# Kernel tuning notes

Measured on AMD Instinct MI355X. Metric: run time of the kernel, lower is better.

The kernel has to match this reference:

```python
import jax, jax.numpy as jnp
from jax import lax
import numpy as np

EPS = 1e-5
DN = ('NCHW', 'OIHW', 'NCHW')
# Sum of the four Sobel-like kernels used in sobel_conv2d (conv is linear, so
# summing four depthwise convs == one depthwise conv with the summed kernel).
SOBEL_SUM = jnp.array([[2., 4., 4.], [-2., 0., 2.], [-4., -4., -2.]], dtype=jnp.float32)


def conv_bn_relu(x, w, b, g, be, m, v, pad):
    y = lax.conv_general_dilated(x, w, (1, 1), [(pad, pad), (pad, pad)], dimension_numbers=DN)
    y = y + b[None, :, None, None]
    inv = g * lax.rsqrt(v + EPS)
    y = (y - m[None, :, None, None]) * inv[None, :, None, None] + be[None, :, None, None]
    return jax.nn.relu(y)


def sobel_depthwise(x):
    C = x.shape[1]
    k = jnp.broadcast_to(SOBEL_SUM[None, None], (C, 1, 3, 3))
    return lax.conv_general_dilated(x, k, (1, 1), [(1, 1), (1, 1)],
                                    dimension_numbers=DN, feature_group_count=C)


def setup_inputs() -> dict:
    key = jax.random.key(0)
    ks = jax.random.split(key, 20)
    B, Cin, H, W = 16, 64, 128, 128
    Co = 256  # out_channels
    d = {'input_f': jax.random.normal(ks[0], (B, Cin, H, W), jnp.float32)}

    def bn(i, c):
        return (jax.random.normal(ks[i], (c,), jnp.float32) * 0.1 + 1.0,  # gamma
                jax.random.normal(ks[i + 1], (c,), jnp.float32) * 0.1,    # beta
                jax.random.normal(ks[i + 2], (c,), jnp.float32) * 0.1,    # running mean
                jax.random.uniform(ks[i + 3], (c,), jnp.float32, 0.5, 1.5))  # running var

    d['w1'] = jax.random.normal(ks[1], (Co, Cin, 1, 1), jnp.float32) * (1.0 / np.sqrt(Cin))
    d['b1'] = jnp.zeros((Co,), jnp.float32)
    d['g1'], d['be1'], d['m1'], d['v1'] = bn(2, Co)
    d['w2'] = jax.random.normal(ks[6], (Co // 2, Co, 3, 3), jnp.float32) * (1.0 / np.sqrt(Co * 9))
    d['b2'] = jnp.zeros((Co // 2,), jnp.float32)
    d['g2'], d['be2'], d['m2'], d['v2'] = bn(7, Co // 2)
    d['w3'] = jax.random.normal(ks[11], (Co // 4, Co // 2, 3, 3), jnp.float32) * (1.0 / np.sqrt(Co // 2 * 9))
    d['b3'] = jnp.zeros((Co // 4,), jnp.float32)
    d['g3'], d['be3'], d['m3'], d['v3'] = bn(12, Co // 4)
    return d


def reference(input_f, w1, b1, g1, be1, m1, v1, w2, b2, g2, be2, m2, v2,
              w3, b3, g3, be3, m3, v3):
    c1 = conv_bn_relu(input_f, w1, b1, g1, be1, m1, v1, pad=0)  # [B,256,H,W]
    c2 = conv_bn_relu(c1, w2, b2, g2, be2, m2, v2, pad=1)       # [B,128,H,W]
    edge = sobel_depthwise(c2)                                   # [B,128,H,W]
    c3 = conv_bn_relu(edge, w3, b3, g3, be3, m3, v3, pad=1)     # [B,64,H,W]
    return jnp.concatenate([input_f, c3], axis=1)                # [B,128,H,W]
```

## Files before the change

kernel.cpp:

```cpp
#include <hip/hip_runtime.h>

#define HW 16384
#define EPSF 1e-5f

typedef __attribute__((ext_vector_type(8))) short s8v;
typedef __attribute__((ext_vector_type(16))) float f16v;

__device__ __forceinline__ ushort f2b(float f) {
    union { float f; unsigned u; } v; v.f = f;
    return (ushort)((v.u + 0x7FFFu + ((v.u >> 16) & 1u)) >> 16);
}
__device__ __forceinline__ float b2f(ushort h) {
    union { unsigned u; float f; } v; v.u = ((unsigned)h) << 16; return v.f;
}


__global__ void bn_prep(const float* __restrict__ b1, const float* __restrict__ g1,
                        const float* __restrict__ be1, const float* __restrict__ m1,
                        const float* __restrict__ v1,
                        const float* __restrict__ b2, const float* __restrict__ g2,
                        const float* __restrict__ be2, const float* __restrict__ m2,
                        const float* __restrict__ v2,
                        const float* __restrict__ b3, const float* __restrict__ g3,
                        const float* __restrict__ be3, const float* __restrict__ m3,
                        const float* __restrict__ v3,
                        float* __restrict__ ws) {
    int t = threadIdx.x;
    if (t < 256) { float a = g1[t] * rsqrtf(v1[t] + EPSF); ws[t] = a;       ws[256 + t] = (b1[t] - m1[t]) * a + be1[t]; }
    if (t < 128) { float a = g2[t] * rsqrtf(v2[t] + EPSF); ws[512 + t] = a; ws[640 + t] = (b2[t] - m2[t]) * a + be2[t]; }
    if (t < 64)  { float a = g3[t] * rsqrtf(v3[t] + EPSF); ws[768 + t] = a; ws[832 + t] = (b3[t] - m3[t]) * a + be3[t]; }
}

__global__ __launch_bounds__(256) void wprep(const float* __restrict__ w2, const float* __restrict__ w3,
                                             const float* __restrict__ w1,
                                             ushort* __restrict__ w2b, ushort* __restrict__ w3b,
                                             ushort* __restrict__ w1b) {
    int t = blockIdx.x * 256 + threadIdx.x;
    if (t < 9 * 128 * 256) {
        int off = t >> 15; int r = t & 32767; int co = r >> 8; int ci = r & 255;
        w2b[t] = f2b(w2[(co * 256 + ci) * 9 + off]);
    }
    t -= 9 * 128 * 256;
    if (t >= 0 && t < 9 * 64 * 128) {
        int off = t >> 13; int r = t & 8191; int co = r >> 7; int ci = r & 127;
        w3b[t] = f2b(w3[(co * 128 + ci) * 9 + off]);
    }
    t -= 9 * 64 * 128;
    if (t >= 0 && t < 256 * 64) {
        w1b[t] = f2b(w1[t]);
    }
}

__global__ __launch_bounds__(256) void copy_in_k(const float* __restrict__ x, float* __restrict__ out) {
    size_t i = (size_t)blockIdx.x * 256 + threadIdx.x;
    size_t b = i >> 18;
    size_t r = i & 262143;
    ((float4*)out)[b * (size_t)(128 * HW / 4) + r] = ((const float4*)x)[i];
}

__global__ __launch_bounds__(256, 2)
void conv1_mfma(const float* __restrict__ x, const ushort* __restrict__ w1b,
                const float* __restrict__ alpha, const float* __restrict__ beta,
                ushort* __restrict__ c1u, int b0) {
    __shared__ __align__(16) ushort sW[256][72];
    const int tid = threadIdx.x;
    const int lane = tid & 63;
    const int wid = tid >> 6;
    const int l31 = lane & 31;
    const int l5 = lane >> 5;
    const int bz = blockIdx.x >> 7;
    const int y  = blockIdx.x & 127;
    const int px = wid * 32 + l31;

#pragma unroll
    for (int it = 0; it < 8; ++it) {
        const int idx = it * 256 + tid;
        const int co = idx >> 3, cig = idx & 7;
        *(int4*)&sW[co][cig * 8] = *(const int4*)&w1b[co * 64 + cig * 8];
    }

    const float* xp = x + ((size_t)(b0 + bz) * 64 + l5 * 8) * HW + y * 128 + px;
    float xv[32];
#pragma unroll
    for (int s = 0; s < 4; ++s)
#pragma unroll
        for (int j = 0; j < 8; ++j)
            xv[s * 8 + j] = xp[(size_t)(s * 16 + j) * HW];

    union { ushort u[8]; s8v v; } hf[4], lf[4];
#pragma unroll
    for (int s = 0; s < 4; ++s)
#pragma unroll
        for (int j = 0; j < 8; ++j) {
            union { float f; unsigned u; } t0; t0.f = xv[s * 8 + j];
            hf[s].u[j] = (ushort)(t0.u >> 16);
            union { unsigned u; float f; } t1; t1.u = t0.u & 0xFFFF0000u;
            lf[s].u[j] = f2b(t0.f - t1.f);
        }

    f16v acc[8];
#pragma unroll
    for (int ct = 0; ct < 8; ++ct) acc[ct] = (f16v)(0.0f);

    __syncthreads();
#pragma unroll
    for (int s = 0; s < 4; ++s) {
#pragma unroll
        for (int ct = 0; ct < 8; ++ct) {
            const s8v af = *(const s8v*)&sW[ct * 32 + l31][s * 16 + l5 * 8];
            acc[ct] = __builtin_amdgcn_mfma_f32_32x32x16_bf16(af, hf[s].v, acc[ct], 0, 0, 0);
            acc[ct] = __builtin_amdgcn_mfma_f32_32x32x16_bf16(af, lf[s].v, acc[ct], 0, 0, 0);
        }
    }

    const int piece = y >> 6;
    const size_t base = (size_t)(2 * bz + piece) * 4194304 + (size_t)(y & 63) * 128 * 256;
#pragma unroll
    for (int ct = 0; ct < 8; ++ct) {
#pragma unroll
        for (int rg = 0; rg < 4; ++rg) {
            const int co0 = ct * 32 + rg * 8 + l5 * 4;
            const float4 av = *(const float4*)&alpha[co0];
            const float4 bv = *(const float4*)&beta[co0];
            ushort4 o;
            o.x = f2b(fmaxf(acc[ct][rg * 4 + 0] * av.x + bv.x, 0.f));
            o.y = f2b(fmaxf(acc[ct][rg * 4 + 1] * av.y + bv.y, 0.f));
            o.z = f2b(fmaxf(acc[ct][rg * 4 + 2] * av.z + bv.z, 0.f));
            o.w = f2b(fmaxf(acc[ct][rg * 4 + 3] * av.w + bv.w, 0.f));
            *(ushort4*)&c1u[base + (size_t)px * 256 + co0] = o;
        }
    }
}

__global__ __launch_bounds__(256, 2)
void conv2_mfma(const ushort* __restrict__ c1u, const ushort* __restrict__ wb,
                const float* __restrict__ alpha, const float* __restrict__ beta,
                ushort* __restrict__ ybf, int b0) {
    constexpr int CI = 256, CO = 128, MT = 2;
    __shared__ __align__(16) ushort sX[2][130][40];
    __shared__ __align__(16) ushort sW[3][CO][40];
    const int tid = threadIdx.x;
    const int lane = tid & 63;
    const int wid = tid >> 6;
    const int wm = wid & 1;
    const int wr = wid >> 1;
    const int l31 = lane & 31;
    const int l5 = lane >> 5;
    const int bz = blockIdx.x >> 6;
    const int y0 = (blockIdx.x & 63) * 2;

    f16v acc[MT][4];
#pragma unroll
    for (int mt = 0; mt < MT; ++mt)
#pragma unroll
        for (int nt = 0; nt < 4; ++nt) acc[mt][nt] = (f16v)(0.0f);

    if (tid < 128) {
        int r = tid >> 6, rem = tid & 63;
        int p = (rem < 32) ? 0 : 129;
        sX[r][p][rem & 31] = 0;
    }

    for (int dy = 0; dy < 3; ++dy) {
        for (int cc = 0; cc < CI; cc += 32) {
            __syncthreads();
#pragma unroll
            for (int it = 0; it < 4; ++it) {
                const int idx = it * 256 + tid;
                const int r = idx >> 9, xx = (idx >> 2) & 127, cig = idx & 3;
                const int yy = y0 + r + dy - 1;
                int4 v = make_int4(0, 0, 0, 0);
                if ((unsigned)yy < 128u) {
                    const size_t base = (size_t)(2 * bz + (yy >> 6)) * 4194304;
                    v = *(const int4*)&c1u[base + (((yy & 63) * 128 + xx) * 256 + cc + cig * 8)];
                }
                *(int4*)&sX[r][xx + 1][cig * 8] = v;
            }
#pragma unroll
            for (int it = 0; it < 6; ++it) {
                const int idx = it * 256 + tid;
                const int dxs = idx >> 9;
                const int r = idx & 511;
                const int co = r >> 2, cig = r & 3;
                *(int4*)&sW[dxs][co][cig * 8] =
                    *(const int4*)&wb[((size_t)((dy * 3 + dxs) * CO) + co) * CI + cc + cig * 8];
            }
            __syncthreads();
#pragma unroll
            for (int dx = 0; dx < 3; ++dx) {
#pragma unroll
                for (int kh = 0; kh < 2; ++kh) {
                    s8v af[MT], bfr[4];
#pragma unroll
                    for (int mt = 0; mt < MT; ++mt)
                        af[mt] = *(const s8v*)&sW[dx][wm * 64 + mt * 32 + l31][kh * 16 + l5 * 8];
#pragma unroll
                    for (int nt = 0; nt < 4; ++nt)
                        bfr[nt] = *(const s8v*)&sX[wr][nt * 32 + l31 + dx][kh * 16 + l5 * 8];
#pragma unroll
                    for (int mt = 0; mt < MT; ++mt)
#pragma unroll
                        for (int nt = 0; nt < 4; ++nt)
                            acc[mt][nt] = __builtin_amdgcn_mfma_f32_32x32x16_bf16(
                                af[mt], bfr[nt], acc[mt][nt], 0, 0, 0);
                }
            }
        }
    }
    const int yy = y0 + wr;
    const size_t cb2 = (size_t)(b0 + bz) * 4194304 + 2097152;
#pragma unroll
    for (int mt = 0; mt < MT; ++mt) {
#pragma unroll
        for (int nt = 0; nt < 4; ++nt) {
            const int xx = nt * 32 + l31;
#pragma unroll
            for (int rg = 0; rg < 4; ++rg) {
                const int co0 = wm * 64 + mt * 32 + rg * 8 + l5 * 4;
                const float4 av = *(const float4*)&alpha[co0];
                const float4 bv = *(const float4*)&beta[co0];
                ushort4 o;
                o.x = f2b(fmaxf(acc[mt][nt][rg * 4 + 0] * av.x + bv.x, 0.f));
                o.y = f2b(fmaxf(acc[mt][nt][rg * 4 + 1] * av.y + bv.y, 0.f));
                o.z = f2b(fmaxf(acc[mt][nt][rg * 4 + 2] * av.z + bv.z, 0.f));
                o.w = f2b(fmaxf(acc[mt][nt][rg * 4 + 3] * av.w + bv.w, 0.f));
                *(ushort4*)&ybf[cb2 + ((size_t)yy * 128 + xx) * 128 + co0] = o;
            }
        }
    }
}

__global__ __launch_bounds__(256)
void sobel_nhwc(const ushort* __restrict__ outu, ushort* __restrict__ edgeu) {
    const int tid = threadIdx.x;
    const int cg = tid & 15;
    const int xl = tid >> 4;
    const int xblk = blockIdx.x & 7;
    const int y = (blockIdx.x >> 3) & 127;
    const int b = blockIdx.x >> 10;
    const int x = xblk * 16 + xl;
    const size_t cb2 = (size_t)b * 4194304 + 2097152;
    const size_t eb = (size_t)b * 4194304;
    float acc[8];
#pragma unroll
    for (int j = 0; j < 8; ++j) acc[j] = 0.f;
    const float cf[9] = {2.f, 4.f, 4.f, -2.f, 0.f, 2.f, -4.f, -4.f, -2.f};
#pragma unroll
    for (int t = 0; t < 9; ++t) {
        if (t == 4) continue;
        const int yy = y + (t / 3) - 1, xx = x + (t % 3) - 1;
        if ((unsigned)yy < 128u && (unsigned)xx < 128u) {
            union { int4 v; ushort s[8]; } u;
            u.v = *(const int4*)&outu[cb2 + ((size_t)yy * 128 + xx) * 128 + cg * 8];
            const float c = cf[t];
#pragma unroll
            for (int j = 0; j < 8; ++j) acc[j] += c * b2f(u.s[j]);
        }
    }
    union { ushort s[8]; int4 v; } o;
#pragma unroll
    for (int j = 0; j < 8; ++j) o.s[j] = f2b(acc[j]);
    *(int4*)&edgeu[eb + ((size_t)y * 128 + x) * 128 + cg * 8] = o.v;
}

__global__ __launch_bounds__(256, 2)
void conv3_mfma(const ushort* __restrict__ edgeu, const ushort* __restrict__ wb,
                const float* __restrict__ alpha, const float* __restrict__ beta,
                float* __restrict__ out) {
    constexpr int CI = 128, CO = 64;
    __shared__ __align__(16) ushort sX[2][130][72];
    __shared__ __align__(16) ushort sW[3][CO][72];
    const int tid = threadIdx.x;
    const int lane = tid & 63;
    const int wid = tid >> 6;
    const int wm = wid & 1;
    const int wr = wid >> 1;
    const int l31 = lane & 31;
    const int l5 = lane >> 5;
    const int b = blockIdx.x >> 6;
    const int y0 = (blockIdx.x & 63) * 2;
    const size_t eb = (size_t)b * 4194304;

    f16v acc[4];
#pragma unroll
    for (int nt = 0; nt < 4; ++nt) acc[nt] = (f16v)(0.0f);

    {
        int r = tid >> 7, rem = tid & 127;
        int p = (rem < 64) ? 0 : 129;
        sX[r][p][rem & 63] = 0;
    }

    for (int dy = 0; dy < 3; ++dy) {
        for (int cc = 0; cc < CI; cc += 64) {
            __syncthreads();
#pragma unroll
            for (int it = 0; it < 8; ++it) {
                const int idx = it * 256 + tid;
                const int r = idx >> 10, xx = (idx >> 3) & 127, cig = idx & 7;
                const int yy = y0 + r + dy - 1;
                int4 v = make_int4(0, 0, 0, 0);
                if ((unsigned)yy < 128u)
                    v = *(const int4*)&edgeu[eb + ((size_t)yy * 128 + xx) * CI + cc + cig * 8];
                *(int4*)&sX[r][xx + 1][cig * 8] = v;
            }
#pragma unroll
            for (int it = 0; it < 6; ++it) {
                const int idx = it * 256 + tid;
                const int dxs = idx >> 9;
                const int r = idx & 511;
                const int co = r >> 3, cig = r & 7;
                *(int4*)&sW[dxs][co][cig * 8] =
                    *(const int4*)&wb[((size_t)((dy * 3 + dxs) * CO) + co) * CI + cc + cig * 8];
            }
            __syncthreads();
#pragma unroll
            for (int dx = 0; dx < 3; ++dx) {
#pragma unroll
                for (int kh = 0; kh < 4; ++kh) {
                    const s8v af = *(const s8v*)&sW[dx][wm * 32 + l31][kh * 16 + l5 * 8];
                    s8v bfr[4];
#pragma unroll
                    for (int nt = 0; nt < 4; ++nt)
                        bfr[nt] = *(const s8v*)&sX[wr][nt * 32 + l31 + dx][kh * 16 + l5 * 8];
#pragma unroll
                    for (int nt = 0; nt < 4; ++nt)
                        acc[nt] = __builtin_amdgcn_mfma_f32_32x32x16_bf16(af, bfr[nt], acc[nt], 0, 0, 0);
                }
            }
        }
    }
    const int yy = y0 + wr;
#pragma unroll
    for (int nt = 0; nt < 4; ++nt) {
        const int xx = nt * 32 + l31;
#pragma unroll
        for (int rg = 0; rg < 4; ++rg) {
            const int co0 = wm * 32 + rg * 8 + l5 * 4;
            const float4 av = *(const float4*)&alpha[co0];
            const float4 bv = *(const float4*)&beta[co0];
            const size_t base = ((size_t)b * 128 + 64 + co0) * HW + yy * 128 + xx;
            out[base]          = fmaxf(acc[nt][rg * 4 + 0] * av.x + bv.x, 0.f);
            out[base + HW]     = fmaxf(acc[nt][rg * 4 + 1] * av.y + bv.y, 0.f);
            out[base + 2 * HW] = fmaxf(acc[nt][rg * 4 + 2] * av.z + bv.z, 0.f);
            out[base + 3 * HW] = fmaxf(acc[nt][rg * 4 + 3] * av.w + bv.w, 0.f);
        }
    }
}

extern "C" void kernel_launch(void* const* d_in, const int* in_sizes, int n_in,
                              void* d_out, int out_size, void* d_ws, size_t ws_size,
                              hipStream_t stream) {
    const float* input = (const float*)d_in[0];
    const float* w1 = (const float*)d_in[1];
    const float* b1 = (const float*)d_in[2];
    const float* g1 = (const float*)d_in[3];
    const float* be1 = (const float*)d_in[4];
    const float* m1 = (const float*)d_in[5];
    const float* v1 = (const float*)d_in[6];
    const float* w2 = (const float*)d_in[7];
    const float* b2 = (const float*)d_in[8];
    const float* g2 = (const float*)d_in[9];
    const float* be2 = (const float*)d_in[10];
    const float* m2 = (const float*)d_in[11];
    const float* v2 = (const float*)d_in[12];
    const float* w3 = (const float*)d_in[13];
    const float* b3 = (const float*)d_in[14];
    const float* g3 = (const float*)d_in[15];
    const float* be3 = (const float*)d_in[16];
    const float* m3 = (const float*)d_in[17];
    const float* v3 = (const float*)d_in[18];
    float* ws = (float*)d_ws;
    float* out = (float*)d_out;
    ushort* outu = (ushort*)d_out;

    float* A1 = ws;        float* B1 = ws + 256;
    float* A2 = ws + 512;  float* B2 = ws + 640;
    float* A3 = ws + 768;  float* B3 = ws + 832;

    char* wsb = (char*)d_ws;
    ushort* w1b = (ushort*)(wsb + 4096);
    ushort* w2b = (ushort*)(wsb + 4096 + 32768);
    ushort* w3b = (ushort*)(wsb + 4096 + 32768 + 589824);

    bn_prep<<<1, 256, 0, stream>>>(b1, g1, be1, m1, v1, b2, g2, be2, m2, v2,
                                   b3, g3, be3, m3, v3, ws);
    wprep<<<1505, 256, 0, stream>>>(w2, w3, w1, w2b, w3b, w1b);

    for (int b0 = 0; b0 < 16; b0 += 8) {
        conv1_mfma<<<1024, 256, 0, stream>>>(input, w1b, A1, B1, outu, b0);
        conv2_mfma<<<512, 256, 0, stream>>>(outu, w2b, A2, B2, outu, b0);
    }
    sobel_nhwc<<<16384, 256, 0, stream>>>(outu, outu);
    conv3_mfma<<<1024, 256, 0, stream>>>(outu, w3b, A3, B3, out);
    copy_in_k<<<16384, 256, 0, stream>>>(input, out);
}
```

Baseline: 552.7 us.

## Split conv2 output channels across blocks and shrink conv3 K-chunk for occupancy

Conv2 now gives each block half of the output channels (64), which doubles the grid to 1024 blocks, halves the accumulator registers and LDS weight tile, and raises launch bounds to 4 blocks per CU. Conv3 drops its K-chunk from 64 to 32 channels to shrink LDS and also targets 4 blocks per CU. Both kernels remap block indices so that neighbouring blocks are spread across XCDs. In exchange, conv2 loads each input tile twice (once per channel half), and both kernels hit more barrier and sync iterations for the same work.

```diff
diff --git a/kernel.cpp b/kernel.cpp
--- a/kernel.cpp
+++ b/kernel.cpp
@@ -132,13 +132,13 @@
     }
 }
 
-__global__ __launch_bounds__(256, 2)
+__global__ __launch_bounds__(256, 4)
 void conv2_mfma(const ushort* __restrict__ c1u, const ushort* __restrict__ wb,
                 const float* __restrict__ alpha, const float* __restrict__ beta,
                 ushort* __restrict__ ybf, int b0) {
-    constexpr int CI = 256, CO = 128, MT = 2;
+    constexpr int CI = 256, CO = 128;
     __shared__ __align__(16) ushort sX[2][130][40];
-    __shared__ __align__(16) ushort sW[3][CO][40];
+    __shared__ __align__(16) ushort sW[3][64][40];
     const int tid = threadIdx.x;
     const int lane = tid & 63;
     const int wid = tid >> 6;
@@ -146,14 +146,14 @@
     const int wr = wid >> 1;
     const int l31 = lane & 31;
     const int l5 = lane >> 5;
-    const int bz = blockIdx.x >> 6;
-    const int y0 = (blockIdx.x & 63) * 2;
-
-    f16v acc[MT][4];
-#pragma unroll
-    for (int mt = 0; mt < MT; ++mt)
-#pragma unroll
-        for (int nt = 0; nt < 4; ++nt) acc[mt][nt] = (f16v)(0.0f);
+    const int lid = (blockIdx.x & 7) * 128 + (blockIdx.x >> 3);
+    const int bz  = lid >> 7;
+    const int y0  = ((lid >> 1) & 63) * 2;
+    const int coh = (lid & 1) * 64;
+
+    f16v acc[4];
+#pragma unroll
+    for (int nt = 0; nt < 4; ++nt) acc[nt] = (f16v)(0.0f);
 
     if (tid < 128) {
         int r = tid >> 6, rem = tid & 63;
@@ -177,32 +177,24 @@
                 *(int4*)&sX[r][xx + 1][cig * 8] = v;
             }
 #pragma unroll
-            for (int it = 0; it < 6; ++it) {
-                const int idx = it * 256 + tid;
-                const int dxs = idx >> 9;
-                const int r = idx & 511;
-                const int co = r >> 2, cig = r & 3;
-                *(int4*)&sW[dxs][co][cig * 8] =
-                    *(const int4*)&wb[((size_t)((dy * 3 + dxs) * CO) + co) * CI + cc + cig * 8];
+            for (int it = 0; it < 3; ++it) {
+                const int co = tid >> 2, cig = tid & 3;
+                *(int4*)&sW[it][co][cig * 8] =
+                    *(const int4*)&wb[((size_t)((dy * 3 + it) * CO) + coh + co) * CI + cc + cig * 8];
             }
             __syncthreads();
 #pragma unroll
             for (int dx = 0; dx < 3; ++dx) {
 #pragma unroll
                 for (int kh = 0; kh < 2; ++kh) {
-                    s8v af[MT], bfr[4];
-#pragma unroll
-                    for (int mt = 0; mt < MT; ++mt)
-                        af[mt] = *(const s8v*)&sW[dx][wm * 64 + mt * 32 + l31][kh * 16 + l5 * 8];
+                    const s8v af = *(const s8v*)&sW[dx][wm * 32 + l31][kh * 16 + l5 * 8];
+                    s8v bfr[4];
 #pragma unroll
                     for (int nt = 0; nt < 4; ++nt)
                         bfr[nt] = *(const s8v*)&sX[wr][nt * 32 + l31 + dx][kh * 16 + l5 * 8];
 #pragma unroll
-                    for (int mt = 0; mt < MT; ++mt)
-#pragma unroll
-                        for (int nt = 0; nt < 4; ++nt)
-                            acc[mt][nt] = __builtin_amdgcn_mfma_f32_32x32x16_bf16(
-                                af[mt], bfr[nt], acc[mt][nt], 0, 0, 0);
+                    for (int nt = 0; nt < 4; ++nt)
+                        acc[nt] = __builtin_amdgcn_mfma_f32_32x32x16_bf16(af, bfr[nt], acc[nt], 0, 0, 0);
                 }
             }
         }
@@ -210,22 +202,19 @@
     const int yy = y0 + wr;
     const size_t cb2 = (size_t)(b0 + bz) * 4194304 + 2097152;
 #pragma unroll
-    for (int mt = 0; mt < MT; ++mt) {
-#pragma unroll
-        for (int nt = 0; nt < 4; ++nt) {
-            const int xx = nt * 32 + l31;
-#pragma unroll
-            for (int rg = 0; rg < 4; ++rg) {
-                const int co0 = wm * 64 + mt * 32 + rg * 8 + l5 * 4;
-                const float4 av = *(const float4*)&alpha[co0];
-                const float4 bv = *(const float4*)&beta[co0];
-                ushort4 o;
-                o.x = f2b(fmaxf(acc[mt][nt][rg * 4 + 0] * av.x + bv.x, 0.f));
-                o.y = f2b(fmaxf(acc[mt][nt][rg * 4 + 1] * av.y + bv.y, 0.f));
-                o.z = f2b(fmaxf(acc[mt][nt][rg * 4 + 2] * av.z + bv.z, 0.f));
-                o.w = f2b(fmaxf(acc[mt][nt][rg * 4 + 3] * av.w + bv.w, 0.f));
-                *(ushort4*)&ybf[cb2 + ((size_t)yy * 128 + xx) * 128 + co0] = o;
-            }
+    for (int nt = 0; nt < 4; ++nt) {
+        const int xx = nt * 32 + l31;
+#pragma unroll
+        for (int rg = 0; rg < 4; ++rg) {
+            const int co0 = coh + wm * 32 + rg * 8 + l5 * 4;
+            const float4 av = *(const float4*)&alpha[co0];
+            const float4 bv = *(const float4*)&beta[co0];
+            ushort4 o;
+            o.x = f2b(fmaxf(acc[nt][rg * 4 + 0] * av.x + bv.x, 0.f));
+            o.y = f2b(fmaxf(acc[nt][rg * 4 + 1] * av.y + bv.y, 0.f));
+            o.z = f2b(fmaxf(acc[nt][rg * 4 + 2] * av.z + bv.z, 0.f));
+            o.w = f2b(fmaxf(acc[nt][rg * 4 + 3] * av.w + bv.w, 0.f));
+            *(ushort4*)&ybf[cb2 + ((size_t)yy * 128 + xx) * 128 + co0] = o;
         }
     }
 }
@@ -263,13 +252,13 @@
     *(int4*)&edgeu[eb + ((size_t)y * 128 + x) * 128 + cg * 8] = o.v;
 }
 
-__global__ __launch_bounds__(256, 2)
+__global__ __launch_bounds__(256, 4)
 void conv3_mfma(const ushort* __restrict__ edgeu, const ushort* __restrict__ wb,
                 const float* __restrict__ alpha, const float* __restrict__ beta,
                 float* __restrict__ out) {
     constexpr int CI = 128, CO = 64;
-    __shared__ __align__(16) ushort sX[2][130][72];
-    __shared__ __align__(16) ushort sW[3][CO][72];
+    __shared__ __align__(16) ushort sX[2][130][40];
+    __shared__ __align__(16) ushort sW[3][64][40];
     const int tid = threadIdx.x;
     const int lane = tid & 63;
     const int wid = tid >> 6;
@@ -277,27 +266,28 @@
     const int wr = wid >> 1;
     const int l31 = lane & 31;
     const int l5 = lane >> 5;
-    const int b = blockIdx.x >> 6;
-    const int y0 = (blockIdx.x & 63) * 2;
+    const int lid = (blockIdx.x & 7) * 128 + (blockIdx.x >> 3);
+    const int b = lid >> 6;
+    const int y0 = (lid & 63) * 2;
     const size_t eb = (size_t)b * 4194304;
 
     f16v acc[4];
 #pragma unroll
     for (int nt = 0; nt < 4; ++nt) acc[nt] = (f16v)(0.0f);
 
-    {
-        int r = tid >> 7, rem = tid & 127;
-        int p = (rem < 64) ? 0 : 129;
-        sX[r][p][rem & 63] = 0;
+    if (tid < 128) {
+        int r = tid >> 6, rem = tid & 63;
+        int p = (rem < 32) ? 0 : 129;
+        sX[r][p][rem & 31] = 0;
     }
 
     for (int dy = 0; dy < 3; ++dy) {
-        for (int cc = 0; cc < CI; cc += 64) {
+        for (int cc = 0; cc < CI; cc += 32) {
             __syncthreads();
 #pragma unroll
-            for (int it = 0; it < 8; ++it) {
+            for (int it = 0; it < 4; ++it) {
                 const int idx = it * 256 + tid;
-                const int r = idx >> 10, xx = (idx >> 3) & 127, cig = idx & 7;
+                const int r = idx >> 9, xx = (idx >> 2) & 127, cig = idx & 3;
                 const int yy = y0 + r + dy - 1;
                 int4 v = make_int4(0, 0, 0, 0);
                 if ((unsigned)yy < 128u)
@@ -305,19 +295,16 @@
                 *(int4*)&sX[r][xx + 1][cig * 8] = v;
             }
 #pragma unroll
-            for (int it = 0; it < 6; ++it) {
-                const int idx = it * 256 + tid;
-                const int dxs = idx >> 9;
-                const int r = idx & 511;
-                const int co = r >> 3, cig = r & 7;
-                *(int4*)&sW[dxs][co][cig * 8] =
-                    *(const int4*)&wb[((size_t)((dy * 3 + dxs) * CO) + co) * CI + cc + cig * 8];
+            for (int it = 0; it < 3; ++it) {
+                const int co = tid >> 2, cig = tid & 3;
+                *(int4*)&sW[it][co][cig * 8] =
+                    *(const int4*)&wb[((size_t)((dy * 3 + it) * CO) + co) * CI + cc + cig * 8];
             }
             __syncthreads();
 #pragma unroll
             for (int dx = 0; dx < 3; ++dx) {
 #pragma unroll
-                for (int kh = 0; kh < 4; ++kh) {
+                for (int kh = 0; kh < 2; ++kh) {
                     const s8v af = *(const s8v*)&sW[dx][wm * 32 + l31][kh * 16 + l5 * 8];
                     s8v bfr[4];
 #pragma unroll
@@ -389,7 +376,7 @@
 
     for (int b0 = 0; b0 < 16; b0 += 8) {
         conv1_mfma<<<1024, 256, 0, stream>>>(input, w1b, A1, B1, outu, b0);
-        conv2_mfma<<<512, 256, 0, stream>>>(outu, w2b, A2, B2, outu, b0);
+        conv2_mfma<<<1024, 256, 0, stream>>>(outu, w2b, A2, B2, outu, b0);
     }
     sobel_nhwc<<<16384, 256, 0, stream>>>(outu, outu);
     conv3_mfma<<<1024, 256, 0, stream>>>(outu, w3b, A3, B3, out);
```

New measurement: 594.5 us. 1.08x slower.

## Prefetch conv2 tiles into registers and stage conv1 output through LDS

Applied to the files above, without the earlier changes.

conv2_mfma now software-pipelines its K loop: global loads for the next (dy, channel-chunk) stage go into registers while MFMAs run on the current LDS tile, then get written to LDS after a barrier. This hides global load latency behind compute, at the cost of more registers (ten int4 per thread) under launch_bounds(256,2). The conv1 epilogue also stages its bf16 outputs in shared memory (reusing sW) and writes them back as coalesced 16-byte rows instead of scattered 8-byte stores, which adds extra barriers.

```diff
diff --git a/kernel.cpp b/kernel.cpp
--- a/kernel.cpp
+++ b/kernel.cpp
@@ -113,21 +113,35 @@
         }
     }
 
+    ushort* sT = &sW[0][0];
     const int piece = y >> 6;
     const size_t base = (size_t)(2 * bz + piece) * 4194304 + (size_t)(y & 63) * 128 * 256;
 #pragma unroll
-    for (int ct = 0; ct < 8; ++ct) {
-#pragma unroll
-        for (int rg = 0; rg < 4; ++rg) {
-            const int co0 = ct * 32 + rg * 8 + l5 * 4;
-            const float4 av = *(const float4*)&alpha[co0];
-            const float4 bv = *(const float4*)&beta[co0];
-            ushort4 o;
-            o.x = f2b(fmaxf(acc[ct][rg * 4 + 0] * av.x + bv.x, 0.f));
-            o.y = f2b(fmaxf(acc[ct][rg * 4 + 1] * av.y + bv.y, 0.f));
-            o.z = f2b(fmaxf(acc[ct][rg * 4 + 2] * av.z + bv.z, 0.f));
-            o.w = f2b(fmaxf(acc[ct][rg * 4 + 3] * av.w + bv.w, 0.f));
-            *(ushort4*)&c1u[base + (size_t)px * 256 + co0] = o;
+    for (int p = 0; p < 2; ++p) {
+        __syncthreads();
+#pragma unroll
+        for (int c4 = 0; c4 < 4; ++c4) {
+            const int ct = p * 4 + c4;
+#pragma unroll
+            for (int rg = 0; rg < 4; ++rg) {
+                const int co = c4 * 32 + rg * 8 + l5 * 4;
+                const float4 av = *(const float4*)&alpha[p * 128 + co];
+                const float4 bv = *(const float4*)&beta[p * 128 + co];
+                ushort4 o;
+                o.x = f2b(fmaxf(acc[ct][rg * 4 + 0] * av.x + bv.x, 0.f));
+                o.y = f2b(fmaxf(acc[ct][rg * 4 + 1] * av.y + bv.y, 0.f));
+                o.z = f2b(fmaxf(acc[ct][rg * 4 + 2] * av.z + bv.z, 0.f));
+                o.w = f2b(fmaxf(acc[ct][rg * 4 + 3] * av.w + bv.w, 0.f));
+                *(ushort4*)&sT[px * 136 + co] = o;
+            }
+        }
+        __syncthreads();
+#pragma unroll
+        for (int it = 0; it < 8; ++it) {
+            const int idx = it * 256 + tid;
+            const int pxx = idx >> 4, c16 = idx & 15;
+            const int4 v = *(const int4*)&sT[pxx * 136 + c16 * 8];
+            *(int4*)&c1u[base + (size_t)pxx * 256 + p * 128 + c16 * 8] = v;
         }
     }
 }
@@ -161,52 +175,84 @@
         sX[r][p][rem & 31] = 0;
     }
 
-    for (int dy = 0; dy < 3; ++dy) {
-        for (int cc = 0; cc < CI; cc += 32) {
+    int4 xv[4], wv[6];
+
+#define C2_LOADS(S) {                                                          \
+        const int dy_ = (S) >> 3, cc_ = ((S) & 7) * 32;                        \
+        _Pragma("unroll")                                                      \
+        for (int it = 0; it < 4; ++it) {                                       \
+            const int idx = it * 256 + tid;                                    \
+            const int r = idx >> 9, xx = (idx >> 2) & 127, cig = idx & 3;      \
+            const int yy = y0 + r + dy_ - 1;                                   \
+            int4 v = make_int4(0, 0, 0, 0);                                    \
+            if ((unsigned)yy < 128u) {                                         \
+                const size_t gb = (size_t)(2 * bz + (yy >> 6)) * 4194304;      \
+                v = *(const int4*)&c1u[gb + (((yy & 63) * 128 + xx) * 256 + cc_ + cig * 8)]; \
+            }                                                                  \
+            xv[it] = v;                                                        \
+        }                                                                      \
+        _Pragma("unroll")                                                      \
+        for (int it = 0; it < 6; ++it) {                                       \
+            const int idx = it * 256 + tid;                                    \
+            const int dxs = idx >> 9;                                          \
+            const int r = idx & 511;                                           \
+            const int co = r >> 2, cig = r & 3;                                \
+            wv[it] = *(const int4*)&wb[((size_t)((dy_ * 3 + dxs) * CO) + co) * CI + cc_ + cig * 8]; \
+        }                                                                      \
+    }
+
+#define C2_WRITES() {                                                          \
+        _Pragma("unroll")                                                      \
+        for (int it = 0; it < 4; ++it) {                                       \
+            const int idx = it * 256 + tid;                                    \
+            const int r = idx >> 9, xx = (idx >> 2) & 127, cig = idx & 3;      \
+            *(int4*)&sX[r][xx + 1][cig * 8] = xv[it];                          \
+        }                                                                      \
+        _Pragma("unroll")                                                      \
+        for (int it = 0; it < 6; ++it) {                                       \
+            const int idx = it * 256 + tid;                                    \
+            const int dxs = idx >> 9;                                          \
+            const int r = idx & 511;                                           \
+            const int co = r >> 2, cig = r & 3;                                \
+            *(int4*)&sW[dxs][co][cig * 8] = wv[it];                            \
+        }                                                                      \
+    }
+
+    C2_LOADS(0);
+    __syncthreads();
+    C2_WRITES();
+    __syncthreads();
+
+    for (int s = 0; s < 24; ++s) {
+        if (s < 23) C2_LOADS(s + 1);
+#pragma unroll
+        for (int dx = 0; dx < 3; ++dx) {
+#pragma unroll
+            for (int kh = 0; kh < 2; ++kh) {
+                s8v af[MT], bfr[4];
+#pragma unroll
+                for (int mt = 0; mt < MT; ++mt)
+                    af[mt] = *(const s8v*)&sW[dx][wm * 64 + mt * 32 + l31][kh * 16 + l5 * 8];
+#pragma unroll
+                for (int nt = 0; nt < 4; ++nt)
+                    bfr[nt] = *(const s8v*)&sX[wr][nt * 32 + l31 + dx][kh * 16 + l5 * 8];
+#pragma unroll
+                for (int mt = 0; mt < MT; ++mt)
+#pragma unroll
+                    for (int nt = 0; nt < 4; ++nt)
+                        acc[mt][nt] = __builtin_amdgcn_mfma_f32_32x32x16_bf16(
+                            af[mt], bfr[nt], acc[mt][nt], 0, 0, 0);
+            }
+        }
+        if (s < 23) {
             __syncthreads();
-#pragma unroll
-            for (int it = 0; it < 4; ++it) {
-                const int idx = it * 256 + tid;
-                const int r = idx >> 9, xx = (idx >> 2) & 127, cig = idx & 3;
-                const int yy = y0 + r + dy - 1;
-                int4 v = make_int4(0, 0, 0, 0);
-                if ((unsigned)yy < 128u) {
-                    const size_t base = (size_t)(2 * bz + (yy >> 6)) * 4194304;
-                    v = *(const int4*)&c1u[base + (((yy & 63) * 128 + xx) * 256 + cc + cig * 8)];
-                }
-                *(int4*)&sX[r][xx + 1][cig * 8] = v;
-            }
-#pragma unroll
-            for (int it = 0; it < 6; ++it) {
-                const int idx = it * 256 + tid;
-                const int dxs = idx >> 9;
-                const int r = idx & 511;
-                const int co = r >> 2, cig = r & 3;
-                *(int4*)&sW[dxs][co][cig * 8] =
-                    *(const int4*)&wb[((size_t)((dy * 3 + dxs) * CO) + co) * CI + cc + cig * 8];
-            }
+            C2_WRITES();
             __syncthreads();
-#pragma unroll
-            for (int dx = 0; dx < 3; ++dx) {
-#pragma unroll
-                for (int kh = 0; kh < 2; ++kh) {
-                    s8v af[MT], bfr[4];
-#pragma unroll
-                    for (int mt = 0; mt < MT; ++mt)
-                        af[mt] = *(const s8v*)&sW[dx][wm * 64 + mt * 32 + l31][kh * 16 + l5 * 8];
-#pragma unroll
-                    for (int nt = 0; nt < 4; ++nt)
-                        bfr[nt] = *(const s8v*)&sX[wr][nt * 32 + l31 + dx][kh * 16 + l5 * 8];
-#pragma unroll
-                    for (int mt = 0; mt < MT; ++mt)
-#pragma unroll
-                        for (int nt = 0; nt < 4; ++nt)
-                            acc[mt][nt] = __builtin_amdgcn_mfma_f32_32x32x16_bf16(
-                                af[mt], bfr[nt], acc[mt][nt], 0, 0, 0);
-                }
-            }
-        }
-    }
+        }
+    }
+#undef C2_LOADS
+#undef C2_WRITES
+
     const int yy = y0 + wr;
     const size_t cb2 = (size_t)(b0 + bz) * 4194304 + 2097152;
 #pragma unroll
```

New measurement: 597.7 us. 8.1% more time.
